# Kernel tuning notes

Measured on AMD Instinct MI355X. Metric: run time of the kernel, lower is better.

## Reference

```python
import math
import jax, jax.numpy as jnp
import numpy as np

N, H, E, K = 8192, 2048, 8, 2
CF = 1.25


def setup_inputs() -> dict:
    key = jax.random.key(0)
    ks = jax.random.split(key, 5)
    s1 = 1.0 / math.sqrt(H)
    s2 = 1.0 / math.sqrt(2 * H)
    return {
        "tokens": jax.random.normal(ks[0], (N, H), jnp.float32),
        "Wr": jax.random.normal(ks[1], (E, H), jnp.float32) * s1,   # router: logits = x @ Wr.T + br
        "br": jnp.zeros((E,), jnp.float32),
        "W1": jax.random.normal(ks[2], (E, H, 2 * H), jnp.float32) * s1,
        "b1": jnp.zeros((E, 2 * H), jnp.float32),
        "W2": jax.random.normal(ks[3], (E, 2 * H, H), jnp.float32) * s2,
        "b2": jnp.zeros((E, H), jnp.float32),
    }


def reference(tokens, Wr, br, W1, b1, W2, b2):
    n = tokens.shape[0]
    cap = max(1, math.ceil(CF * n / E))  # per-expert capacity (static)

    # --- router + top-k ---
    logits = tokens @ Wr.T + br                         # [N, E]
    scores, expert_ids = jax.lax.top_k(logits, K)       # [N, K]
    probs = jax.nn.softmax(scores, axis=-1)

    # --- flatten dispatches and sort by expert (stable, like the torch code) ---
    flat_e = expert_ids.reshape(-1)                     # [N*K]
    flat_t = jnp.repeat(jnp.arange(n), K)               # [N*K]
    flat_s = probs.reshape(-1).astype(tokens.dtype)     # [N*K]
    order = jnp.argsort(flat_e)                         # jnp.argsort is stable
    se, st, ss = flat_e[order], flat_t[order], flat_s[order]

    # --- capacity-limited gather: fixed [E, cap] index grid ---
    seg_start = jnp.searchsorted(se, jnp.arange(E))     # [E] first slot of each expert segment
    counts = jnp.bincount(se, length=E)                 # [E] tokens routed to each expert
    slot = jnp.arange(cap)
    idx = jnp.clip(seg_start[:, None] + slot[None, :], 0, n * K - 1)  # [E, cap]
    valid = slot[None, :] < jnp.minimum(counts, cap)[:, None]          # [E, cap]
    tok_idx = st[idx]                                   # [E, cap] source token ids
    w = jnp.where(valid, ss[idx], 0.0)[..., None]       # [E, cap, 1] combine weights (0 => dropped)

    # --- grouped per-expert FFN (GEMM over [E, cap, H]) ---
    x = tokens[tok_idx]                                 # [E, cap, H]
    h = jax.nn.gelu(jnp.einsum('ech,ehf->ecf', x, W1) + b1[:, None, :], approximate=False)
    y = jnp.einsum('ecf,efh->ech', h, W2) + b2[:, None, :]

    # --- weighted scatter-add combine ---
    out = jnp.zeros_like(tokens).at[tok_idx.reshape(-1)].add((y * w).reshape(-1, tokens.shape[-1]))
    return out
```

## Files before the change

kernel.cpp:

```cpp
#include <hip/hip_runtime.h>
#include <hip/hip_bf16.h>
#include <math.h>

#define NTOK 8192
#define HDIM 2048
#define NEXP 8
#define TOPK 2
#define CAP  1280
#define FF   4096
#define BK   32

typedef float  f32x4  __attribute__((ext_vector_type(4)));
typedef __bf16 bf16x8 __attribute__((ext_vector_type(8)));

typedef __attribute__((address_space(1))) const unsigned int gas_u32;
typedef __attribute__((address_space(3))) unsigned int las_u32;

__device__ __forceinline__ void gload16(const void* g, void* l) {
    __builtin_amdgcn_global_load_lds((gas_u32*)g, (las_u32*)l, 16, 0, 0);
}

__device__ __forceinline__ ushort f2bf(float f) {
    union { float f; unsigned u; } c; c.f = f;
    unsigned u = c.u;
    unsigned r = (u + 0x7FFFu + ((u >> 16) & 1u)) >> 16;
    return (ushort)r;
}
__device__ __forceinline__ float bf2f(ushort h) {
    union { unsigned u; float f; } c; c.u = ((unsigned)h) << 16;
    return c.f;
}

__global__ void k_convert(const float* __restrict__ src, ushort* __restrict__ dst) {
    int i = (blockIdx.x * 256 + threadIdx.x) * 8;
    float4 a = *(const float4*)(src + i);
    float4 b = *(const float4*)(src + i + 4);
    uint4 o;
    o.x = (unsigned)f2bf(a.x) | ((unsigned)f2bf(a.y) << 16);
    o.y = (unsigned)f2bf(a.z) | ((unsigned)f2bf(a.w) << 16);
    o.z = (unsigned)f2bf(b.x) | ((unsigned)f2bf(b.y) << 16);
    o.w = (unsigned)f2bf(b.z) | ((unsigned)f2bf(b.w) << 16);
    *(uint4*)(dst + i) = o;
}

__global__ void k_router(const float* __restrict__ tokens, const float* __restrict__ Wr,
                         const float* __restrict__ br, int* __restrict__ eids,
                         float* __restrict__ probs) {
    int wave = threadIdx.x >> 6, lane = threadIdx.x & 63;
    int t = blockIdx.x * 4 + wave;
    const float* tp = tokens + (size_t)t * HDIM;
    double acc[NEXP];
    #pragma unroll
    for (int e = 0; e < NEXP; ++e) acc[e] = 0.0;
    for (int j = 0; j < HDIM / 64; ++j) {
        float x = tp[j * 64 + lane];
        #pragma unroll
        for (int e = 0; e < NEXP; ++e)
            acc[e] += (double)x * (double)Wr[e * HDIM + j * 64 + lane];
    }
    #pragma unroll
    for (int e = 0; e < NEXP; ++e) {
        #pragma unroll
        for (int off = 32; off; off >>= 1) acc[e] += __shfl_xor(acc[e], off, 64);
    }
    if (lane == 0) {
        float lg[NEXP];
        #pragma unroll
        for (int e = 0; e < NEXP; ++e) lg[e] = (float)acc[e] + br[e];
        int e0 = 0; float s0 = lg[0];
        #pragma unroll
        for (int e = 1; e < NEXP; ++e) if (lg[e] > s0) { s0 = lg[e]; e0 = e; }
        int e1 = -1; float s1 = -1e30f;
        #pragma unroll
        for (int e = 0; e < NEXP; ++e) if (e != e0 && lg[e] > s1) { s1 = lg[e]; e1 = e; }
        float ex = expf(s1 - s0);
        float den = 1.f + ex;
        eids[t * 2] = e0; eids[t * 2 + 1] = e1;
        probs[t * 2] = 1.f / den; probs[t * 2 + 1] = ex / den;
    }
}

__global__ void k_assign(const int* __restrict__ eids, int* __restrict__ tok_map,
                         int* __restrict__ dest) {
    __shared__ int cnt[64][NEXP];
    int l = threadIdx.x;
    for (int i = l; i < NEXP * CAP; i += 64) tok_map[i] = 0;
    int c[NEXP];
    #pragma unroll
    for (int e = 0; e < NEXP; ++e) c[e] = 0;
    const int base = l * 256;
    for (int i = 0; i < 256; ++i) {
        int ee = eids[base + i];
        #pragma unroll
        for (int e = 0; e < NEXP; ++e) c[e] += (ee == e);
    }
    #pragma unroll
    for (int e = 0; e < NEXP; ++e) cnt[l][e] = c[e];
    __syncthreads();
    if (l < NEXP) {
        int run = 0;
        for (int b = 0; b < 64; ++b) { int v = cnt[b][l]; cnt[b][l] = run; run += v; }
    }
    __syncthreads();
    int off[NEXP];
    #pragma unroll
    for (int e = 0; e < NEXP; ++e) off[e] = cnt[l][e];
    for (int i = 0; i < 256; ++i) {
        int d = base + i;
        int ee = eids[d];
        int r = -1;
        #pragma unroll
        for (int e = 0; e < NEXP; ++e) { bool m = (ee == e); if (m) r = off[e]; off[e] += m; }
        if (r < CAP) { tok_map[ee * CAP + r] = d >> 1; dest[d] = ee * CAP + r; }
        else dest[d] = -1;
    }
}

__global__ __launch_bounds__(256) void k_transpose(const float* __restrict__ src,
                                                   ushort* __restrict__ dst,
                                                   int Kd, int Nd) {
    __shared__ float tl[64][65];
    int e = blockIdx.z;
    int k0 = blockIdx.x * 64, n0 = blockIdx.y * 64;
    const float* s = src + (size_t)e * Kd * Nd;
    ushort* d = dst + (size_t)e * Kd * Nd;
    int tid = threadIdx.x;
    #pragma unroll
    for (int i = 0; i < 4; ++i) {
        int flat = (i * 256 + tid) * 4;
        int kk = flat >> 6, nn = flat & 63;
        float4 v = *(const float4*)(s + (size_t)(k0 + kk) * Nd + n0 + nn);
        tl[kk][nn] = v.x; tl[kk][nn + 1] = v.y; tl[kk][nn + 2] = v.z; tl[kk][nn + 3] = v.w;
    }
    __syncthreads();
    #pragma unroll
    for (int g = 0; g < 4; ++g) {
        int flat = g * 1024 + tid * 4;
        int nn = flat >> 6, kk = flat & 63;
        uint2 o;
        o.x = (unsigned)f2bf(tl[kk][nn])     | ((unsigned)f2bf(tl[kk + 1][nn]) << 16);
        o.y = (unsigned)f2bf(tl[kk + 2][nn]) | ((unsigned)f2bf(tl[kk + 3][nn]) << 16);
        *(uint2*)(d + (size_t)(n0 + nn) * Kd + k0 + kk) = o;
    }
}

template<bool DOGELU, bool GATHER>
__global__ __launch_bounds__(256) void k_gemm(const ushort* __restrict__ A,
                                              const int* __restrict__ tmap,
                                              const ushort* __restrict__ B,
                                              const float* __restrict__ bias,
                                              ushort* __restrict__ C,
                                              int Kd, int Nd) {
    __shared__ ushort As[128 * BK];
    __shared__ ushort Bs[128 * BK];
    const int tid = threadIdx.x;
    const int lane = tid & 63;
    const int wave = tid >> 6;
    const int wr = wave >> 1, wc = wave & 1;
    const int e = blockIdx.z;
    const int bm0 = blockIdx.y * 128, bn0 = blockIdx.x * 128;

    const ushort* Be = B + (size_t)e * Nd * Kd;
    const int R  = tid >> 2;
    const int kc = (tid & 3) * 8;
    int ra0, ra1;
    if (GATHER) { ra0 = tmap[e * CAP + bm0 + R]; ra1 = tmap[e * CAP + bm0 + R + 64]; }
    else        { ra0 = e * CAP + bm0 + R;       ra1 = e * CAP + bm0 + R + 64; }
    const ushort* pa0 = A + (size_t)ra0 * Kd + kc;
    const ushort* pa1 = A + (size_t)ra1 * Kd + kc;
    const ushort* pb0 = Be + (size_t)(bn0 + R) * Kd + kc;
    const ushort* pb1 = Be + (size_t)(bn0 + R + 64) * Kd + kc;
    char* lA0 = (char*)As + wave * 1024;
    char* lA1 = (char*)As + 4096 + wave * 1024;
    char* lB0 = (char*)Bs + wave * 1024;
    char* lB1 = (char*)Bs + 4096 + wave * 1024;

    const int fr = lane & 15, kg = (lane >> 4) * 8;
    f32x4 acc[4][4] = {};

    for (int k0 = 0; k0 < Kd; k0 += BK) {
        __syncthreads();
        gload16(pa0 + k0, lA0);
        gload16(pa1 + k0, lA1);
        gload16(pb0 + k0, lB0);
        gload16(pb1 + k0, lB1);
        __syncthreads();
        bf16x8 af[4], bfr[4];
        #pragma unroll
        for (int mi = 0; mi < 4; ++mi)
            af[mi] = *(const bf16x8*)(As + (wr * 64 + mi * 16 + fr) * BK + kg);
        #pragma unroll
        for (int ni = 0; ni < 4; ++ni)
            bfr[ni] = *(const bf16x8*)(Bs + (wc * 64 + ni * 16 + fr) * BK + kg);
        #pragma unroll
        for (int mi = 0; mi < 4; ++mi)
            #pragma unroll
            for (int ni = 0; ni < 4; ++ni)
                acc[mi][ni] = __builtin_amdgcn_mfma_f32_16x16x32_bf16(af[mi], bfr[ni],
                                                                      acc[mi][ni], 0, 0, 0);
    }

    const float* be = bias + e * Nd;
    ushort* Ce = C + (size_t)e * CAP * Nd;
    const int rl = (lane >> 4) * 4, cl = lane & 15;
    #pragma unroll
    for (int mi = 0; mi < 4; ++mi) {
        #pragma unroll
        for (int ni = 0; ni < 4; ++ni) {
            #pragma unroll
            for (int r = 0; r < 4; ++r) {
                int gr = bm0 + wr * 64 + mi * 16 + rl + r;
                int gc = bn0 + wc * 64 + ni * 16 + cl;
                float v = acc[mi][ni][r] + be[gc];
                if (DOGELU) v = 0.5f * v * (1.f + erff(v * 0.70710678118654752f));
                Ce[(size_t)gr * Nd + gc] = f2bf(v);
            }
        }
    }
}

__global__ void k_combine(const ushort* __restrict__ Y, const int* __restrict__ dest,
                          const float* __restrict__ probs, float* __restrict__ out) {
    int t = blockIdx.x;
    int h0 = threadIdx.x * 8;
    int d0 = dest[t * 2], d1 = dest[t * 2 + 1];
    float p0 = d0 >= 0 ? probs[t * 2] : 0.f;
    float p1 = d1 >= 0 ? probs[t * 2 + 1] : 0.f;
    int r0 = d0 >= 0 ? d0 : 0, r1 = d1 >= 0 ? d1 : 0;
    uint4 a = *(const uint4*)(Y + (size_t)r0 * HDIM + h0);
    uint4 b = *(const uint4*)(Y + (size_t)r1 * HDIM + h0);
    float4 o0, o1;
    o0.x = p0 * bf2f(a.x & 0xffff) + p1 * bf2f(b.x & 0xffff);
    o0.y = p0 * bf2f(a.x >> 16)    + p1 * bf2f(b.x >> 16);
    o0.z = p0 * bf2f(a.y & 0xffff) + p1 * bf2f(b.y & 0xffff);
    o0.w = p0 * bf2f(a.y >> 16)    + p1 * bf2f(b.y >> 16);
    o1.x = p0 * bf2f(a.z & 0xffff) + p1 * bf2f(b.z & 0xffff);
    o1.y = p0 * bf2f(a.z >> 16)    + p1 * bf2f(b.z >> 16);
    o1.z = p0 * bf2f(a.w & 0xffff) + p1 * bf2f(b.w & 0xffff);
    o1.w = p0 * bf2f(a.w >> 16)    + p1 * bf2f(b.w >> 16);
    float* op = out + (size_t)t * HDIM + h0;
    *(float4*)op = o0;
    *(float4*)(op + 4) = o1;
}

extern "C" void kernel_launch(void* const* d_in, const int* in_sizes, int n_in,
                              void* d_out, int out_size, void* d_ws, size_t ws_size,
                              hipStream_t stream) {
    const float* tokens = (const float*)d_in[0];
    const float* Wr     = (const float*)d_in[1];
    const float* br     = (const float*)d_in[2];
    const float* W1     = (const float*)d_in[3];
    const float* b1     = (const float*)d_in[4];
    const float* W2     = (const float*)d_in[5];
    const float* b2     = (const float*)d_in[6];
    float* out = (float*)d_out;
    char* ws = (char*)d_ws;

    int*    eids    = (int*)(ws);
    float*  probs   = (float*)(ws + 65536);
    int*    tok_map = (int*)(ws + 131072);
    int*    dest    = (int*)(ws + 172032);
    size_t off = 1u << 20;
    ushort* TbY = (ushort*)(ws + off);
    off += 41943040;
    ushort* Hm  = (ushort*)(ws + off);
    off += 83886080;
    ushort* WT  = (ushort*)(ws + off);
    (void)in_sizes; (void)n_in; (void)out_size; (void)ws_size;

    k_convert<<<dim3(NTOK * HDIM / 2048), 256, 0, stream>>>(tokens, TbY);
    k_router<<<dim3(NTOK / 4), 256, 0, stream>>>(tokens, Wr, br, eids, probs);
    k_assign<<<dim3(1), 64, 0, stream>>>(eids, tok_map, dest);
    k_transpose<<<dim3(HDIM / 64, FF / 64, NEXP), 256, 0, stream>>>(W1, WT, HDIM, FF);
    k_gemm<true, true><<<dim3(FF / 128, CAP / 128, NEXP), 256, 0, stream>>>(
        TbY, tok_map, WT, b1, Hm, HDIM, FF);
    k_transpose<<<dim3(FF / 64, HDIM / 64, NEXP), 256, 0, stream>>>(W2, WT, FF, HDIM);
    k_gemm<false, false><<<dim3(HDIM / 128, CAP / 128, NEXP), 256, 0, stream>>>(
        Hm, nullptr, WT, b2, TbY, FF, HDIM);
    k_combine<<<dim3(NTOK), 256, 0, stream>>>(TbY, dest, probs, out);
}
```

Before: 818.7 us.

## Rewrite expert GEMM with 256x256 tiles, double-buffered swizzled LDS, and interleaved MFMA schedule

Replaces the single-buffered 128x128 BK=32 GEMM with a 512-thread, 256x256-tile kernel. It uses BK=64 and double-buffered direct global-to-LDS loads into a 128KB LDS buffer with XOR swizzling. The K loop interleaves async staging of the next tiles with MFMA phases gated by explicit s_barrier and vmcnt waits, and raises wave priority around the MFMA bursts. The aim is to hide global load latency and increase operand reuse per LDS read. In exchange, each CU holds fewer blocks and the grid is coarser, which can leave a wave-quantization tail on the second GEMM.

```diff
diff --git a/kernel.cpp b/kernel.cpp
--- a/kernel.cpp
+++ b/kernel.cpp
@@ -8,7 +8,6 @@
 #define TOPK 2
 #define CAP  1280
 #define FF   4096
-#define BK   32
 
 typedef float  f32x4  __attribute__((ext_vector_type(4)));
 typedef __bf16 bf16x8 __attribute__((ext_vector_type(8)));
@@ -144,74 +143,135 @@
     }
 }
 
+#define BAR()   asm volatile("s_barrier" ::: "memory")
+#define VMC4()  asm volatile("s_waitcnt vmcnt(4)" ::: "memory")
+
 template<bool DOGELU, bool GATHER>
-__global__ __launch_bounds__(256) void k_gemm(const ushort* __restrict__ A,
-                                              const int* __restrict__ tmap,
-                                              const ushort* __restrict__ B,
-                                              const float* __restrict__ bias,
-                                              ushort* __restrict__ C,
-                                              int Kd, int Nd) {
-    __shared__ ushort As[128 * BK];
-    __shared__ ushort Bs[128 * BK];
-    const int tid = threadIdx.x;
+__global__ __launch_bounds__(512, 2) void k_gemm(const ushort* __restrict__ A,
+                                                 const int* __restrict__ tmap,
+                                                 const ushort* __restrict__ B,
+                                                 const float* __restrict__ bias,
+                                                 ushort* __restrict__ C,
+                                                 int Kd, int Nd) {
+    __shared__ char lds[131072];
+    const int tid  = threadIdx.x;
     const int lane = tid & 63;
     const int wave = tid >> 6;
-    const int wr = wave >> 1, wc = wave & 1;
+    const int wr = wave >> 2, wc = wave & 3;
     const int e = blockIdx.z;
-    const int bm0 = blockIdx.y * 128, bn0 = blockIdx.x * 128;
-
-    const ushort* Be = B + (size_t)e * Nd * Kd;
-    const int R  = tid >> 2;
-    const int kc = (tid & 3) * 8;
-    int ra0, ra1;
-    if (GATHER) { ra0 = tmap[e * CAP + bm0 + R]; ra1 = tmap[e * CAP + bm0 + R + 64]; }
-    else        { ra0 = e * CAP + bm0 + R;       ra1 = e * CAP + bm0 + R + 64; }
-    const ushort* pa0 = A + (size_t)ra0 * Kd + kc;
-    const ushort* pa1 = A + (size_t)ra1 * Kd + kc;
-    const ushort* pb0 = Be + (size_t)(bn0 + R) * Kd + kc;
-    const ushort* pb1 = Be + (size_t)(bn0 + R + 64) * Kd + kc;
-    char* lA0 = (char*)As + wave * 1024;
-    char* lA1 = (char*)As + 4096 + wave * 1024;
-    char* lB0 = (char*)Bs + wave * 1024;
-    char* lB1 = (char*)Bs + 4096 + wave * 1024;
-
-    const int fr = lane & 15, kg = (lane >> 4) * 8;
-    f32x4 acc[4][4] = {};
-
-    for (int k0 = 0; k0 < Kd; k0 += BK) {
-        __syncthreads();
-        gload16(pa0 + k0, lA0);
-        gload16(pa1 + k0, lA1);
-        gload16(pb0 + k0, lB0);
-        gload16(pb1 + k0, lB1);
-        __syncthreads();
-        bf16x8 af[4], bfr[4];
-        #pragma unroll
-        for (int mi = 0; mi < 4; ++mi)
-            af[mi] = *(const bf16x8*)(As + (wr * 64 + mi * 16 + fr) * BK + kg);
-        #pragma unroll
-        for (int ni = 0; ni < 4; ++ni)
-            bfr[ni] = *(const bf16x8*)(Bs + (wc * 64 + ni * 16 + fr) * BK + kg);
-        #pragma unroll
-        for (int mi = 0; mi < 4; ++mi)
+    const int bm0 = blockIdx.y * 256, bn0 = blockIdx.x * 256;
+
+    const int srow = tid >> 3;
+    const int swzc = (tid ^ (tid >> 3)) & 7;
+    const ushort* Be = B + (size_t)e * (size_t)Nd * Kd;
+    const ushort* pa[4]; const ushort* pb[4];
+    #pragma unroll
+    for (int h = 0; h < 2; ++h)
+        #pragma unroll
+        for (int j = 0; j < 2; ++j) {
+            int mrow = bm0 + h * 128 + j * 64 + srow;
+            int arow = GATHER ? tmap[e * CAP + mrow] : (e * CAP + mrow);
+            pa[h * 2 + j] = A  + (size_t)arow * Kd + swzc * 8;
+            pb[h * 2 + j] = Be + (size_t)(bn0 + h * 128 + j * 64 + srow) * Kd + swzc * 8;
+        }
+    const int ldsW = wave * 1024;
+
+    const int fr = lane & 15, kq = lane >> 4;
+    const int x0 = ((kq ^ (fr & 7)) * 16);
+    const int sA = wr * 16384 + fr * 128;
+    const int sB = 65536 + (wc >> 1) * 16384 + ((wc & 1) * 64 + fr) * 128;
+
+    f32x4  acc[8][4] = {};
+    bf16x8 bfr[4][2];
+
+    auto STAGE_A = [&](int b, int kt) {
+        #pragma unroll
+        for (int hj = 0; hj < 4; ++hj)
+            gload16(pa[hj] + (size_t)kt * 64,
+                    lds + b * 32768 + (hj >> 1) * 16384 + (hj & 1) * 8192 + ldsW);
+    };
+    auto STAGE_B = [&](int b, int kt) {
+        #pragma unroll
+        for (int hj = 0; hj < 4; ++hj)
+            gload16(pb[hj] + (size_t)kt * 64,
+                    lds + 65536 + b * 32768 + (hj >> 1) * 16384 + (hj & 1) * 8192 + ldsW);
+    };
+    auto LDA_ = [&](bf16x8 (&af)[4][2], int b, int mh) {
+        #pragma unroll
+        for (int m = 0; m < 4; ++m)
             #pragma unroll
-            for (int ni = 0; ni < 4; ++ni)
-                acc[mi][ni] = __builtin_amdgcn_mfma_f32_16x16x32_bf16(af[mi], bfr[ni],
-                                                                      acc[mi][ni], 0, 0, 0);
+            for (int ks = 0; ks < 2; ++ks)
+                af[m][ks] = *(const bf16x8*)(lds + b * 32768 + sA + (mh * 4 + m) * 2048
+                                             + (x0 ^ (ks << 6)));
+    };
+    auto LDB2 = [&](int b, int nh) {
+        #pragma unroll
+        for (int n = 0; n < 2; ++n)
+            #pragma unroll
+            for (int ks = 0; ks < 2; ++ks)
+                bfr[nh * 2 + n][ks] = *(const bf16x8*)(lds + b * 32768 + sB
+                                                       + (nh * 2 + n) * 2048 + (x0 ^ (ks << 6)));
+    };
+    auto MMA = [&](bf16x8 (&af)[4][2], int mh, int nh) {
+        __builtin_amdgcn_s_setprio(1);
+        #pragma unroll
+        for (int m = 0; m < 4; ++m)
+            #pragma unroll
+            for (int n = 0; n < 2; ++n)
+                #pragma unroll
+                for (int ks = 0; ks < 2; ++ks)
+                    acc[mh * 4 + m][nh * 2 + n] = __builtin_amdgcn_mfma_f32_16x16x32_bf16(
+                        af[m][ks], bfr[nh * 2 + n][ks], acc[mh * 4 + m][nh * 2 + n], 0, 0, 0);
+        __builtin_amdgcn_s_setprio(0);
+    };
+
+    const int NT  = Kd >> 6;
+    const int nt2 = NT >> 1;
+
+    STAGE_A(0, 0); STAGE_B(0, 0); STAGE_B(1, 1);
+    VMC4();
+    BAR();
+
+    for (int it = 0; it < nt2; ++it) {
+        const int kt1  = 2 * it + 1;
+        const int ktN  = min(2 * it + 2, NT - 1);
+        const int ktN1 = min(2 * it + 3, NT - 1);
+        bf16x8 af[4][2];
+        LDA_(af, 0, 0); LDB2(0, 0);
+        STAGE_A(1, kt1);
+        BAR(); MMA(af, 0, 0); BAR();
+        LDB2(0, 1);
+        BAR(); MMA(af, 0, 1); BAR();
+        LDA_(af, 0, 1);
+        STAGE_B(0, ktN);
+        BAR(); MMA(af, 1, 0); BAR();
+        VMC4();
+        BAR(); MMA(af, 1, 1); BAR();
+        LDA_(af, 1, 0); LDB2(1, 0);
+        STAGE_A(0, ktN);
+        BAR(); MMA(af, 0, 0); BAR();
+        LDB2(1, 1);
+        BAR(); MMA(af, 0, 1); BAR();
+        LDA_(af, 1, 1);
+        STAGE_B(1, ktN1);
+        BAR(); MMA(af, 1, 0); BAR();
+        VMC4();
+        BAR(); MMA(af, 1, 1); BAR();
     }
 
     const float* be = bias + e * Nd;
     ushort* Ce = C + (size_t)e * CAP * Nd;
     const int rl = (lane >> 4) * 4, cl = lane & 15;
     #pragma unroll
-    for (int mi = 0; mi < 4; ++mi) {
-        #pragma unroll
-        for (int ni = 0; ni < 4; ++ni) {
+    for (int ni = 0; ni < 4; ++ni) {
+        int gc = bn0 + wc * 64 + ni * 16 + cl;
+        float bv = be[gc];
+        #pragma unroll
+        for (int mi = 0; mi < 8; ++mi) {
             #pragma unroll
             for (int r = 0; r < 4; ++r) {
-                int gr = bm0 + wr * 64 + mi * 16 + rl + r;
-                int gc = bn0 + wc * 64 + ni * 16 + cl;
-                float v = acc[mi][ni][r] + be[gc];
+                int gr = bm0 + wr * 128 + mi * 16 + rl + r;
+                float v = acc[mi][ni][r] + bv;
                 if (DOGELU) v = 0.5f * v * (1.f + erff(v * 0.70710678118654752f));
                 Ce[(size_t)gr * Nd + gc] = f2bf(v);
             }
@@ -272,10 +332,10 @@
     k_router<<<dim3(NTOK / 4), 256, 0, stream>>>(tokens, Wr, br, eids, probs);
     k_assign<<<dim3(1), 64, 0, stream>>>(eids, tok_map, dest);
     k_transpose<<<dim3(HDIM / 64, FF / 64, NEXP), 256, 0, stream>>>(W1, WT, HDIM, FF);
-    k_gemm<true, true><<<dim3(FF / 128, CAP / 128, NEXP), 256, 0, stream>>>(
+    k_gemm<true, true><<<dim3(FF / 256, CAP / 256, NEXP), 512, 0, stream>>>(
         TbY, tok_map, WT, b1, Hm, HDIM, FF);
     k_transpose<<<dim3(FF / 64, HDIM / 64, NEXP), 256, 0, stream>>>(W2, WT, FF, HDIM);
-    k_gemm<false, false><<<dim3(HDIM / 128, CAP / 128, NEXP), 256, 0, stream>>>(
+    k_gemm<false, false><<<dim3(HDIM / 256, CAP / 256, NEXP), 512, 0, stream>>>(
         Hm, nullptr, WT, b2, TbY, FF, HDIM);
     k_combine<<<dim3(NTOK), 256, 0, stream>>>(TbY, dest, probs, out);
 }
```

Measured after the change: 757.5 us. 1.08x faster.

## Triple-buffer GEMM LDS loads with swizzled layout and expert-interleaved block order

Applied to the files above, without the earlier changes.

Replaces the two-barrier single-buffer k-loop in the grouped GEMM with a 3-stage LDS ring: global-to-LDS loads for tile t+2 are issued while tile t is computed, gated by a vmcnt wait and one barrier per iteration. The LDS chunk placement is XOR-swizzled to reduce bank conflicts on fragment reads. The grid is flattened with the expert index in the low bits so concurrent blocks spread across experts. This aims to hide global memory latency and LDS conflicts, at the cost of 48KB LDS per block, which may reduce occupancy, and some redundant loads of the last tile.

```diff
diff --git a/kernel.cpp b/kernel.cpp
--- a/kernel.cpp
+++ b/kernel.cpp
@@ -144,6 +144,9 @@
     }
 }
 
+#define SCHED0() __builtin_amdgcn_sched_barrier(0)
+#define VMC4()   do { asm volatile("s_waitcnt vmcnt(4)" ::: "memory"); } while (0)
+
 template<bool DOGELU, bool GATHER>
 __global__ __launch_bounds__(256) void k_gemm(const ushort* __restrict__ A,
                                               const int* __restrict__ tmap,
@@ -151,18 +154,22 @@
                                               const float* __restrict__ bias,
                                               ushort* __restrict__ C,
                                               int Kd, int Nd) {
-    __shared__ ushort As[128 * BK];
-    __shared__ ushort Bs[128 * BK];
-    const int tid = threadIdx.x;
+    __shared__ __attribute__((aligned(128))) char lds[49152];
+    const int tid  = threadIdx.x;
     const int lane = tid & 63;
     const int wave = tid >> 6;
     const int wr = wave >> 1, wc = wave & 1;
-    const int e = blockIdx.z;
-    const int bm0 = blockIdx.y * 128, bn0 = blockIdx.x * 128;
-
-    const ushort* Be = B + (size_t)e * Nd * Kd;
+    const int NBX = Nd >> 7;
+    const int nbxs = (NBX == 32) ? 5 : 4;
+    const int bid = blockIdx.x;
+    const int e = bid & 7;
+    const int rem = bid >> 3;
+    const int bm0 = (rem >> nbxs) * 128, bn0 = (rem & (NBX - 1)) * 128;
+
+    const ushort* Be = B + (size_t)e * (size_t)Nd * Kd;
     const int R  = tid >> 2;
-    const int kc = (tid & 3) * 8;
+    const int g  = (tid & 3) ^ ((tid >> 4) & 3);
+    const int kc = g * 8;
     int ra0, ra1;
     if (GATHER) { ra0 = tmap[e * CAP + bm0 + R]; ra1 = tmap[e * CAP + bm0 + R + 64]; }
     else        { ra0 = e * CAP + bm0 + R;       ra1 = e * CAP + bm0 + R + 64; }
@@ -170,33 +177,44 @@
     const ushort* pa1 = A + (size_t)ra1 * Kd + kc;
     const ushort* pb0 = Be + (size_t)(bn0 + R) * Kd + kc;
     const ushort* pb1 = Be + (size_t)(bn0 + R + 64) * Kd + kc;
-    char* lA0 = (char*)As + wave * 1024;
-    char* lA1 = (char*)As + 4096 + wave * 1024;
-    char* lB0 = (char*)Bs + wave * 1024;
-    char* lB1 = (char*)Bs + 4096 + wave * 1024;
-
-    const int fr = lane & 15, kg = (lane >> 4) * 8;
+    const int ldsW = wave * 1024;
+
+    auto STAGE = [&](int buf, int kt) {
+        char* d = lds + buf * 16384;
+        gload16(pa0 + kt * BK, d + ldsW);
+        gload16(pa1 + kt * BK, d + 4096 + ldsW);
+        gload16(pb0 + kt * BK, d + 8192 + ldsW);
+        gload16(pb1 + kt * BK, d + 12288 + ldsW);
+    };
+
+    const int fr = lane & 15, kq = lane >> 4;
+    const int cb = (kq ^ ((fr >> 2) & 3)) * 16;
+    int offA[4], offB[4];
+    #pragma unroll
+    for (int mi = 0; mi < 4; ++mi) offA[mi] = (wr * 64 + mi * 16 + fr) * 64 + cb;
+    #pragma unroll
+    for (int ni = 0; ni < 4; ++ni) offB[ni] = 8192 + (wc * 64 + ni * 16 + fr) * 64 + cb;
+
     f32x4 acc[4][4] = {};
-
-    for (int k0 = 0; k0 < Kd; k0 += BK) {
-        __syncthreads();
-        gload16(pa0 + k0, lA0);
-        gload16(pa1 + k0, lA1);
-        gload16(pb0 + k0, lB0);
-        gload16(pb1 + k0, lB1);
-        __syncthreads();
-        bf16x8 af[4], bfr[4];
-        #pragma unroll
-        for (int mi = 0; mi < 4; ++mi)
-            af[mi] = *(const bf16x8*)(As + (wr * 64 + mi * 16 + fr) * BK + kg);
-        #pragma unroll
-        for (int ni = 0; ni < 4; ++ni)
-            bfr[ni] = *(const bf16x8*)(Bs + (wc * 64 + ni * 16 + fr) * BK + kg);
+    const int nt = Kd / BK;
+
+    STAGE(0, 0); STAGE(1, 1);
+    for (int t = 0; t < nt; ++t) {
+        VMC4();
+        __builtin_amdgcn_s_barrier();
+        SCHED0();
+        STAGE((t + 2) % 3, min(t + 2, nt - 1));
+        const char* rb = lds + (t % 3) * 16384;
+        bf16x8 af[4], bf[4];
+        #pragma unroll
+        for (int mi = 0; mi < 4; ++mi) af[mi] = *(const bf16x8*)(rb + offA[mi]);
+        #pragma unroll
+        for (int ni = 0; ni < 4; ++ni) bf[ni] = *(const bf16x8*)(rb + offB[ni]);
         #pragma unroll
         for (int mi = 0; mi < 4; ++mi)
             #pragma unroll
             for (int ni = 0; ni < 4; ++ni)
-                acc[mi][ni] = __builtin_amdgcn_mfma_f32_16x16x32_bf16(af[mi], bfr[ni],
+                acc[mi][ni] = __builtin_amdgcn_mfma_f32_16x16x32_bf16(af[mi], bf[ni],
                                                                       acc[mi][ni], 0, 0, 0);
     }
 
@@ -272,10 +290,10 @@
     k_router<<<dim3(NTOK / 4), 256, 0, stream>>>(tokens, Wr, br, eids, probs);
     k_assign<<<dim3(1), 64, 0, stream>>>(eids, tok_map, dest);
     k_transpose<<<dim3(HDIM / 64, FF / 64, NEXP), 256, 0, stream>>>(W1, WT, HDIM, FF);
-    k_gemm<true, true><<<dim3(FF / 128, CAP / 128, NEXP), 256, 0, stream>>>(
+    k_gemm<true, true><<<dim3((FF / 128) * (CAP / 128) * NEXP), 256, 0, stream>>>(
         TbY, tok_map, WT, b1, Hm, HDIM, FF);
     k_transpose<<<dim3(FF / 64, HDIM / 64, NEXP), 256, 0, stream>>>(W2, WT, FF, HDIM);
-    k_gemm<false, false><<<dim3(HDIM / 128, CAP / 128, NEXP), 256, 0, stream>>>(
+    k_gemm<false, false><<<dim3((HDIM / 128) * (CAP / 128) * NEXP), 256, 0, stream>>>(
         Hm, nullptr, WT, b2, TbY, FF, HDIM);
     k_combine<<<dim3(NTOK), 256, 0, stream>>>(TbY, dest, probs, out);
 }
```

Measured after the change: 751.4 us. -8.2%, faster.
